# Kernel tuning notes

Hardware: AMD Instinct MI355X
Metric: run time of the kernel (lower is better)

Reference implementation:

```python
import jax, jax.numpy as jnp
import numpy as np

B, S, D, H, HID = 8192, 16, 128, 8, 1024
DH = D // H  # 16
GCN, NUMF = 40, 103
EPS = 1e-5

def _make_pe():
    pos = np.arange(S, dtype=np.float64)[:, None]
    i = np.arange(D, dtype=np.float64)[None, :]
    pe = pos / np.power(10000.0, (i // 2 * 2.0) / D)
    pe[:, 0::2] = np.sin(pe[:, 0::2])
    pe[:, 1::2] = np.cos(pe[:, 1::2])
    return jnp.asarray(pe, dtype=jnp.float32)  # [S, D]

PE = _make_pe()

def setup_inputs() -> dict:
    key = jax.random.key(0)
    ks = jax.random.split(key, 16)
    rn = lambda k, shape, s=0.02: (jax.random.normal(k, shape, jnp.float32) * s)
    return {
        "x": jax.random.normal(ks[0], (B, S, D), jnp.float32),
        "gcn_i": jax.random.normal(ks[1], (B, GCN), jnp.float32),
        "num": jax.random.normal(ks[2], (B, NUMF), jnp.float32),
        # two independent encoder layers, params stacked on leading dim
        "Wq": rn(ks[3], (2, D, D)), "bq": jnp.zeros((2, D), jnp.float32),
        "Wk": rn(ks[4], (2, D, D)), "bk": jnp.zeros((2, D), jnp.float32),
        "Wv": rn(ks[5], (2, D, D)), "bv": jnp.zeros((2, D), jnp.float32),
        "Wo": rn(ks[6], (2, D, D)), "bo": jnp.zeros((2, D), jnp.float32),
        "ln1_g": jnp.ones((2, D), jnp.float32), "ln1_b": jnp.zeros((2, D), jnp.float32),
        "W1": rn(ks[7], (2, D, HID)), "b1": jnp.zeros((2, HID), jnp.float32),
        "W2": rn(ks[8], (2, HID, D)), "b2": jnp.zeros((2, D), jnp.float32),
        "ln2_g": jnp.ones((2, D), jnp.float32), "ln2_b": jnp.zeros((2, D), jnp.float32),
        # head
        "Wn": rn(ks[9], (NUMF, D)), "bnum": jnp.zeros((D,), jnp.float32),
        "bn_gamma": jnp.ones((D,), jnp.float32), "bn_beta": jnp.zeros((D,), jnp.float32),
        "Wf": rn(ks[10], (S * D + GCN + D, 1)), "bf": jnp.zeros((1,), jnp.float32),
    }

def _ln(x, g, b):
    m = x.mean(-1, keepdims=True)
    v = ((x - m) ** 2).mean(-1, keepdims=True)
    return (x - m) * jax.lax.rsqrt(v + EPS) * g + b

def reference(x, gcn_i, num, Wq, bq, Wk, bk, Wv, bv, Wo, bo, ln1_g, ln1_b,
              W1, b1, W2, b2, ln2_g, ln2_b, Wn, bnum, bn_gamma, bn_beta, Wf, bf):
    out = x + PE  # positional encoding (dropout = identity in eval)
    scale = DH ** -0.5
    for l in range(2):
        # NOTE: original uses a raw .view(B*H, -1, DH) (no transpose) -- faithful reshape
        q = (out @ Wq[l] + bq[l]).reshape(B * H, S, DH)
        k = (out @ Wk[l] + bk[l]).reshape(B * H, S, DH)
        v = (out @ Wv[l] + bv[l]).reshape(B * H, S, DH)
        attn = jax.nn.softmax(jnp.einsum('nsd,ntd->nst', q, k) * scale, axis=-1)
        ctx = jnp.einsum('nst,ntd->nsd', attn, v).reshape(B, S, D)
        h = _ln(ctx @ Wo[l] + bo[l] + out, ln1_g[l], ln1_b[l])
        ff = jax.nn.relu(h @ W1[l] + b1[l]) @ W2[l] + b2[l]
        out = _ln(ff + h, ln2_g[l], ln2_b[l])
    flat = out.reshape(B, S * D)  # [B, 2048]
    n = num @ Wn + bnum  # [B, 128]
    # BatchNorm1d, training-mode forward (biased batch variance)
    mu = n.mean(0)
    var = ((n - mu) ** 2).mean(0)
    n = (n - mu) * jax.lax.rsqrt(var + EPS) * bn_gamma + bn_beta
    p = jnp.concatenate([flat, gcn_i, n], axis=-1)  # [B, 2216]
    return jax.nn.sigmoid(p @ Wf + bf)
```

## Files before the change

kernel.cpp:

```cpp
#include <hip/hip_runtime.h>
#include <hip/hip_bf16.h>
#include <math.h>

#define B_SZ   8192
#define S_SZ   16
#define D_SZ   128
#define HID_SZ 1024
#define NUMF_SZ 103
#define GCN_SZ 40
#define G_B    4
#define NBLK   (B_SZ / G_B)
#define STRD   136

typedef short bh8 __attribute__((ext_vector_type(8)));
typedef float fx4 __attribute__((ext_vector_type(4)));

__device__ __forceinline__ fx4 mfma16(bh8 a, bh8 b, fx4 c) {
    return __builtin_amdgcn_mfma_f32_16x16x32_bf16(a, b, c, 0, 0, 0);
}

__device__ __forceinline__ unsigned short f2b(float f) {
    unsigned u = __float_as_uint(f);
    return (unsigned short)((u + 0x7fffu + ((u >> 16) & 1u)) >> 16);
}
__device__ __forceinline__ float bu2f(unsigned short u) {
    return __uint_as_float(((unsigned)u) << 16);
}

__global__ __launch_bounds__(256) void prep_weights(
    const float* __restrict__ Wq, const float* __restrict__ Wk,
    const float* __restrict__ Wv, const float* __restrict__ Wo,
    const float* __restrict__ W1, const float* __restrict__ W2,
    unsigned short* __restrict__ WswQ, unsigned short* __restrict__ WswK,
    unsigned short* __restrict__ WswV, unsigned short* __restrict__ WswO,
    unsigned short* __restrict__ Wsw1, unsigned short* __restrict__ Wsw2,
    float* __restrict__ PEt)
{
    int i = blockIdx.x * 256 + threadIdx.x;
    if (i < 2048) {
        int s = i >> 7, c = i & 127;
        float expo = (float)((c >> 1) * 2) * (1.0f / 128.0f);
        float denom = powf(10000.0f, expo);
        float ang = (float)s / denom;
        PEt[i] = (c & 1) ? cosf(ang) : sinf(ang);
    }
    if (i < 2 * 16384) {
        int l = i >> 14, r = i & 16383;
        int nt = r >> 11, ks = (r >> 9) & 3, lane = (r >> 3) & 63, e = r & 7;
        int k = ks * 32 + (lane >> 4) * 8 + e;
        int n = nt * 16 + (lane & 15);
        int s = l * 16384 + k * 128 + n;
        WswQ[i] = f2b(Wq[s]); WswK[i] = f2b(Wk[s]);
        WswV[i] = f2b(Wv[s]); WswO[i] = f2b(Wo[s]);
    }
    {
        int l = i >> 17, r = i & 131071;
        int nt = r >> 11, ks = (r >> 9) & 3, lane = (r >> 3) & 63, e = r & 7;
        int k = ks * 32 + (lane >> 4) * 8 + e;
        int n = nt * 16 + (lane & 15);
        Wsw1[i] = f2b(W1[l * 131072 + k * 1024 + n]);
    }
    {
        int l = i >> 17, r = i & 131071;
        int nt = r >> 14, kt = (r >> 9) & 31, lane = (r >> 3) & 63, e = r & 7;
        int k = kt * 32 + (lane >> 4) * 8 + e;
        int n = nt * 16 + (lane & 15);
        Wsw2[i] = f2b(W2[l * 131072 + k * 128 + n]);
    }
}

__global__ __launch_bounds__(256, 2) void encoder_fused(
    const float* __restrict__ x, const float* __restrict__ gcn,
    const float* __restrict__ bq, const float* __restrict__ bk,
    const float* __restrict__ bv, const float* __restrict__ bo,
    const float* __restrict__ ln1g, const float* __restrict__ ln1b,
    const float* __restrict__ b1, const float* __restrict__ b2p,
    const float* __restrict__ ln2g, const float* __restrict__ ln2b,
    const float* __restrict__ Wf,
    const unsigned short* __restrict__ WswQ, const unsigned short* __restrict__ WswK,
    const unsigned short* __restrict__ WswV, const unsigned short* __restrict__ WswO,
    const unsigned short* __restrict__ Wsw1, const unsigned short* __restrict__ Wsw2,
    const float* __restrict__ PEt,
    float* __restrict__ acc1)
{
    __shared__ unsigned short ACT[64][STRD];
    __shared__ unsigned short Qb[64][STRD];
    __shared__ unsigned short Kb[64][STRD];
    __shared__ unsigned short Vb[64][STRD];
    __shared__ float LNp[64][4][2];
    __shared__ float LNs[64][2];

    const int t = threadIdx.x;
    const int w = t >> 6, lane = t & 63;
    const int q = lane >> 4, ln = lane & 15;
    const int bbase = blockIdx.x * G_B;

    {
        const float4* xb = (const float4*)(x + (size_t)bbase * 2048);
        const float4* pe4 = (const float4*)PEt;
#pragma unroll
        for (int i = 0; i < 8; ++i) {
            int f4 = i * 256 + t;
            float4 xv = xb[f4];
            float4 pv = pe4[f4 & 511];
            int flat = f4 * 4;
            int row = flat >> 7, col = flat & 127;
            ushort4 pk = {f2b(xv.x + pv.x), f2b(xv.y + pv.y),
                          f2b(xv.z + pv.z), f2b(xv.w + pv.w)};
            *(ushort4*)&ACT[row][col] = pk;
        }
    }
    __syncthreads();

    for (int l = 0; l < 2; ++l) {
        {
            bh8 afr[4][4];
#pragma unroll
            for (int mt = 0; mt < 4; ++mt)
#pragma unroll
                for (int ks = 0; ks < 4; ++ks)
                    afr[mt][ks] = *(const bh8*)&ACT[mt * 16 + ln][ks * 32 + q * 8];
            const unsigned short* Wm[3] = {WswQ + l * 16384, WswK + l * 16384, WswV + l * 16384};
            const float* bias3[3] = {bq + l * 128, bk + l * 128, bv + l * 128};
#pragma unroll
            for (int mtx = 0; mtx < 3; ++mtx) {
                unsigned short (*dst)[STRD] = (mtx == 0) ? Qb : (mtx == 1) ? Kb : Vb;
#pragma unroll
                for (int i2 = 0; i2 < 2; ++i2) {
                    int nt = w * 2 + i2;
                    bh8 wfr[4];
#pragma unroll
                    for (int ks = 0; ks < 4; ++ks)
                        wfr[ks] = *(const bh8*)(Wm[mtx] + ((nt * 4 + ks) * 64 + lane) * 8);
                    int n = nt * 16 + ln;
                    float bb = bias3[mtx][n];
#pragma unroll
                    for (int mt = 0; mt < 4; ++mt) {
                        fx4 acc = {0.f, 0.f, 0.f, 0.f};
#pragma unroll
                        for (int ks = 0; ks < 4; ++ks) acc = mfma16(afr[mt][ks], wfr[ks], acc);
#pragma unroll
                        for (int r2 = 0; r2 < 4; ++r2)
                            dst[mt * 16 + q * 4 + r2][n] = f2b(acc[r2] + bb);
                    }
                }
            }
        }
        __syncthreads();

        {
            int base = w * 16;
            int g = lane >> 3, u0 = (lane & 7) * 2;
            float qr[2][16];
#pragma unroll
            for (int h = 0; h < 2; ++h) {
                int u = u0 + h;
                int qsr = base + 2 * g + (u >> 3), qc = (u & 7) * 16;
                bh8 a0 = *(const bh8*)&Qb[qsr][qc];
                bh8 a1 = *(const bh8*)&Qb[qsr][qc + 8];
#pragma unroll
                for (int e = 0; e < 8; ++e) {
                    qr[h][e] = bu2f((unsigned short)a0[e]);
                    qr[h][8 + e] = bu2f((unsigned short)a1[e]);
                }
            }
            float p[2][16];
#pragma unroll
            for (int tp = 0; tp < 16; ++tp) {
                int ksr = base + 2 * g + (tp >> 3), kc = (tp & 7) * 16;
                bh8 k0 = *(const bh8*)&Kb[ksr][kc];
                bh8 k1 = *(const bh8*)&Kb[ksr][kc + 8];
                float d0 = 0.f, d1 = 0.f;
#pragma unroll
                for (int e = 0; e < 8; ++e) {
                    float kv = bu2f((unsigned short)k0[e]);
                    d0 = fmaf(qr[0][e], kv, d0); d1 = fmaf(qr[1][e], kv, d1);
                }
#pragma unroll
                for (int e = 0; e < 8; ++e) {
                    float kv = bu2f((unsigned short)k1[e]);
                    d0 = fmaf(qr[0][8 + e], kv, d0); d1 = fmaf(qr[1][8 + e], kv, d1);
                }
                p[0][tp] = d0 * 0.25f; p[1][tp] = d1 * 0.25f;
            }
#pragma unroll
            for (int h = 0; h < 2; ++h) {
                float mx = -1e30f;
#pragma unroll
                for (int tp = 0; tp < 16; ++tp) mx = fmaxf(mx, p[h][tp]);
                float sum = 0.f;
#pragma unroll
                for (int tp = 0; tp < 16; ++tp) { p[h][tp] = __expf(p[h][tp] - mx); sum += p[h][tp]; }
                float is = 1.0f / sum;
#pragma unroll
                for (int tp = 0; tp < 16; ++tp) p[h][tp] *= is;
            }
            float ctx[2][16];
#pragma unroll
            for (int h = 0; h < 2; ++h)
#pragma unroll
                for (int e = 0; e < 16; ++e) ctx[h][e] = 0.f;
#pragma unroll
            for (int tp = 0; tp < 16; ++tp) {
                int vsr = base + 2 * g + (tp >> 3), vc = (tp & 7) * 16;
                bh8 v0 = *(const bh8*)&Vb[vsr][vc];
                bh8 v1 = *(const bh8*)&Vb[vsr][vc + 8];
#pragma unroll
                for (int e = 0; e < 8; ++e) {
                    float vv = bu2f((unsigned short)v0[e]);
                    ctx[0][e] = fmaf(p[0][tp], vv, ctx[0][e]);
                    ctx[1][e] = fmaf(p[1][tp], vv, ctx[1][e]);
                }
#pragma unroll
                for (int e = 0; e < 8; ++e) {
                    float vv = bu2f((unsigned short)v1[e]);
                    ctx[0][8 + e] = fmaf(p[0][tp], vv, ctx[0][8 + e]);
                    ctx[1][8 + e] = fmaf(p[1][tp], vv, ctx[1][8 + e]);
                }
            }
#pragma unroll
            for (int h = 0; h < 2; ++h) {
                int u = u0 + h;
                int s = base + 2 * g + (u >> 3), dc = (u & 7) * 16;
                bh8 c0, c1;
#pragma unroll
                for (int e = 0; e < 8; ++e) {
                    c0[e] = (short)f2b(ctx[h][e]);
                    c1[e] = (short)f2b(ctx[h][8 + e]);
                }
                *(bh8*)&Qb[s][dc] = c0;
                *(bh8*)&Qb[s][dc + 8] = c1;
            }
        }
        __syncthreads();

        fx4 Cv[2][4];
        {
            bh8 cfr[4][4];
#pragma unroll
            for (int mt = 0; mt < 4; ++mt)
#pragma unroll
                for (int ks = 0; ks < 4; ++ks)
                    cfr[mt][ks] = *(const bh8*)&Qb[mt * 16 + ln][ks * 32 + q * 8];
#pragma unroll
            for (int i2 = 0; i2 < 2; ++i2) {
                int nt = w * 2 + i2, n = nt * 16 + ln;
                bh8 wfr[4];
#pragma unroll
                for (int ks = 0; ks < 4; ++ks)
                    wfr[ks] = *(const bh8*)(WswO + l * 16384 + ((nt * 4 + ks) * 64 + lane) * 8);
                float bb = bo[l * 128 + n];
#pragma unroll
                for (int mt = 0; mt < 4; ++mt) {
                    fx4 acc = {0.f, 0.f, 0.f, 0.f};
#pragma unroll
                    for (int ks = 0; ks < 4; ++ks) acc = mfma16(cfr[mt][ks], wfr[ks], acc);
#pragma unroll
                    for (int r2 = 0; r2 < 4; ++r2)
                        Cv[i2][mt][r2] = acc[r2] + bb +
                            bu2f(ACT[mt * 16 + q * 4 + r2][n]);
                }
            }
        }
#pragma unroll
        for (int mt = 0; mt < 4; ++mt) {
            float s4[4], v4[4];
#pragma unroll
            for (int r2 = 0; r2 < 4; ++r2) {
                float a0 = Cv[0][mt][r2], a1 = Cv[1][mt][r2];
                float s = a0 + a1, v = a0 * a0 + a1 * a1;
#pragma unroll
                for (int m = 1; m < 16; m <<= 1) { s += __shfl_xor(s, m); v += __shfl_xor(v, m); }
                s4[r2] = s; v4[r2] = v;
            }
            if (ln < 8)
                LNp[mt * 16 + q * 4 + (ln >> 1)][w][ln & 1] = (ln & 1) ? v4[ln >> 1] : s4[ln >> 1];
        }
        __syncthreads();
        if (t < 64) {
            float s = LNp[t][0][0] + LNp[t][1][0] + LNp[t][2][0] + LNp[t][3][0];
            float v = LNp[t][0][1] + LNp[t][1][1] + LNp[t][2][1] + LNp[t][3][1];
            float mean = s * (1.0f / 128.0f);
            LNs[t][0] = mean;
            LNs[t][1] = rsqrtf(v * (1.0f / 128.0f) - mean * mean + 1e-5f);
        }
        __syncthreads();
#pragma unroll
        for (int i2 = 0; i2 < 2; ++i2) {
            int n = (w * 2 + i2) * 16 + ln;
            float gg = ln1g[l * 128 + n], be = ln1b[l * 128 + n];
#pragma unroll
            for (int mt = 0; mt < 4; ++mt)
#pragma unroll
                for (int r2 = 0; r2 < 4; ++r2) {
                    int row = mt * 16 + q * 4 + r2;
                    Kb[row][n] = f2b((Cv[i2][mt][r2] - LNs[row][0]) * LNs[row][1] * gg + be);
                }
        }
        __syncthreads();

        bh8 hfr[4][4];
#pragma unroll
        for (int mt = 0; mt < 4; ++mt)
#pragma unroll
            for (int ks = 0; ks < 4; ++ks)
                hfr[mt][ks] = *(const bh8*)&Kb[mt * 16 + ln][ks * 32 + q * 8];
        fx4 f2a[2][4];
#pragma unroll
        for (int i2 = 0; i2 < 2; ++i2)
#pragma unroll
            for (int mt = 0; mt < 4; ++mt) f2a[i2][mt] = fx4{0.f, 0.f, 0.f, 0.f};
        for (int ch = 0; ch < 8; ++ch) {
            bh8 w1fr[2][4];
#pragma unroll
            for (int i2 = 0; i2 < 2; ++i2) {
                int ntg = ch * 8 + w * 2 + i2;
#pragma unroll
                for (int ks = 0; ks < 4; ++ks)
                    w1fr[i2][ks] = *(const bh8*)(Wsw1 + l * 131072 + ((ntg * 4 + ks) * 64 + lane) * 8);
            }
#pragma unroll
            for (int mt = 0; mt < 4; ++mt) {
#pragma unroll
                for (int i2 = 0; i2 < 2; ++i2) {
                    fx4 acc = {0.f, 0.f, 0.f, 0.f};
#pragma unroll
                    for (int ks = 0; ks < 4; ++ks) acc = mfma16(hfr[mt][ks], w1fr[i2][ks], acc);
                    int nl = (w * 2 + i2) * 16 + ln;
                    float bb = b1[l * HID_SZ + ch * 128 + nl];
#pragma unroll
                    for (int r2 = 0; r2 < 4; ++r2) {
                        float vv = acc[r2] + bb;
                        Qb[mt * 16 + q * 4 + r2][nl] = f2b(vv > 0.f ? vv : 0.f);
                    }
                }
            }
            __syncthreads();
            bh8 w2fr[2][4];
#pragma unroll
            for (int i2 = 0; i2 < 2; ++i2)
#pragma unroll
                for (int ks = 0; ks < 4; ++ks)
                    w2fr[i2][ks] = *(const bh8*)(Wsw2 + l * 131072 +
                        (((w * 2 + i2) * 32 + ch * 4 + ks) * 64 + lane) * 8);
#pragma unroll
            for (int mt = 0; mt < 4; ++mt) {
                bh8 ffr[4];
#pragma unroll
                for (int ks = 0; ks < 4; ++ks)
                    ffr[ks] = *(const bh8*)&Qb[mt * 16 + ln][ks * 32 + q * 8];
#pragma unroll
                for (int i2 = 0; i2 < 2; ++i2)
#pragma unroll
                    for (int ks = 0; ks < 4; ++ks)
                        f2a[i2][mt] = mfma16(ffr[ks], w2fr[i2][ks], f2a[i2][mt]);
            }
            __syncthreads();
        }
        fx4 Cv2[2][4];
#pragma unroll
        for (int i2 = 0; i2 < 2; ++i2) {
            int n = (w * 2 + i2) * 16 + ln;
            float bb = b2p[l * 128 + n];
#pragma unroll
            for (int mt = 0; mt < 4; ++mt)
#pragma unroll
                for (int r2 = 0; r2 < 4; ++r2)
                    Cv2[i2][mt][r2] = f2a[i2][mt][r2] + bb +
                        bu2f(Kb[mt * 16 + q * 4 + r2][n]);
        }
#pragma unroll
        for (int mt = 0; mt < 4; ++mt) {
            float s4[4], v4[4];
#pragma unroll
            for (int r2 = 0; r2 < 4; ++r2) {
                float a0 = Cv2[0][mt][r2], a1 = Cv2[1][mt][r2];
                float s = a0 + a1, v = a0 * a0 + a1 * a1;
#pragma unroll
                for (int m = 1; m < 16; m <<= 1) { s += __shfl_xor(s, m); v += __shfl_xor(v, m); }
                s4[r2] = s; v4[r2] = v;
            }
            if (ln < 8)
                LNp[mt * 16 + q * 4 + (ln >> 1)][w][ln & 1] = (ln & 1) ? v4[ln >> 1] : s4[ln >> 1];
        }
        __syncthreads();
        if (t < 64) {
            float s = LNp[t][0][0] + LNp[t][1][0] + LNp[t][2][0] + LNp[t][3][0];
            float v = LNp[t][0][1] + LNp[t][1][1] + LNp[t][2][1] + LNp[t][3][1];
            float mean = s * (1.0f / 128.0f);
            LNs[t][0] = mean;
            LNs[t][1] = rsqrtf(v * (1.0f / 128.0f) - mean * mean + 1e-5f);
        }
        __syncthreads();
#pragma unroll
        for (int i2 = 0; i2 < 2; ++i2) {
            int n = (w * 2 + i2) * 16 + ln;
            float gg = ln2g[l * 128 + n], be = ln2b[l * 128 + n];
#pragma unroll
            for (int mt = 0; mt < 4; ++mt)
#pragma unroll
                for (int r2 = 0; r2 < 4; ++r2) {
                    int row = mt * 16 + q * 4 + r2;
                    ACT[row][n] = f2b((Cv2[i2][mt][r2] - LNs[row][0]) * LNs[row][1] * gg + be);
                }
        }
        __syncthreads();
    }

    {
        int bg = bbase + w;
        float part = 0.f;
        int srow = lane >> 2, c0 = (lane & 3) * 32;
#pragma unroll
        for (int i = 0; i < 4; ++i) {
            bh8 av = *(const bh8*)&ACT[w * 16 + srow][c0 + i * 8];
            int fl = srow * 128 + c0 + i * 8;
#pragma unroll
            for (int e = 0; e < 8; ++e)
                part = fmaf(bu2f((unsigned short)av[e]), Wf[fl + e], part);
        }
        if (lane < GCN_SZ)
            part = fmaf(gcn[(size_t)bg * GCN_SZ + lane], Wf[2048 + lane], part);
#pragma unroll
        for (int off = 32; off; off >>= 1) part += __shfl_xor(part, off);
        if (lane == 0) acc1[bg] = part;
    }
}

__global__ __launch_bounds__(256) void num_stats_kernel(
    const float* __restrict__ num, const float* __restrict__ Wn,
    const float* __restrict__ bnum,
    float* __restrict__ ssum, float* __restrict__ ssq)
{
    __shared__ float NUM[16][NUMF_SZ + 1];
    __shared__ float cred[4][128];
    const int t = threadIdx.x;
    const int b0 = blockIdx.x * 16;
    const int j = t & 127, sg = t >> 7, s0 = sg * 8;

    for (int idx = t; idx < 16 * NUMF_SZ; idx += 256) {
        int r = idx / NUMF_SZ, f = idx - r * NUMF_SZ;
        NUM[r][f] = num[(size_t)(b0 + r) * NUMF_SZ + f];
    }
    __syncthreads();

    float acc[8];
    float bnv = bnum[j];
#pragma unroll
    for (int r = 0; r < 8; ++r) acc[r] = bnv;
    for (int f = 0; f < NUMF_SZ; ++f) {
        float w = Wn[f * 128 + j];
#pragma unroll
        for (int r = 0; r < 8; ++r) acc[r] = fmaf(NUM[s0 + r][f], w, acc[r]);
    }
    float lsum = 0.f, lsq = 0.f;
#pragma unroll
    for (int r = 0; r < 8; ++r) {
        lsum += acc[r];
        lsq = fmaf(acc[r], acc[r], lsq);
    }
    cred[sg][j] = lsum;
    cred[2 + sg][j] = lsq;
    __syncthreads();
    if (sg == 0) atomicAdd(&ssum[j], cred[0][j] + cred[1][j]);
    else         atomicAdd(&ssq[j],  cred[2][j] + cred[3][j]);
}

__global__ __launch_bounds__(128) void final_kernel(
    const float* __restrict__ num, const float* __restrict__ Wn,
    const float* __restrict__ bnum,
    const float* __restrict__ ssum, const float* __restrict__ ssq,
    const float* __restrict__ gamma, const float* __restrict__ beta,
    const float* __restrict__ Wf, const float* __restrict__ bfin,
    const float* __restrict__ acc1, float* __restrict__ out)
{
    const int b = blockIdx.x, jj = threadIdx.x;
    __shared__ float red2[2];
    __shared__ float NUMr[NUMF_SZ];
    if (jj < NUMF_SZ) NUMr[jj] = num[(size_t)b * NUMF_SZ + jj];
    __syncthreads();

    float nv = bnum[jj];
    for (int f = 0; f < NUMF_SZ; ++f)
        nv = fmaf(NUMr[f], Wn[f * 128 + jj], nv);

    float mean = ssum[jj] * (1.0f / (float)B_SZ);
    float var = ssq[jj] * (1.0f / (float)B_SZ) - mean * mean;
    float bnv = (nv - mean) * rsqrtf(var + 1e-5f) * gamma[jj] + beta[jj];
    float v = bnv * Wf[2088 + jj];
#pragma unroll
    for (int o = 32; o; o >>= 1) v += __shfl_down(v, o);
    if ((jj & 63) == 0) red2[jj >> 6] = v;
    __syncthreads();
    if (jj == 0) {
        float z = acc1[b] + red2[0] + red2[1] + bfin[0];
        out[b] = 1.0f / (1.0f + __expf(-z));
    }
}

extern "C" void kernel_launch(void* const* d_in, const int* in_sizes, int n_in,
                              void* d_out, int out_size, void* d_ws, size_t ws_size,
                              hipStream_t stream)
{
    const float* x    = (const float*)d_in[0];
    const float* gcn  = (const float*)d_in[1];
    const float* num  = (const float*)d_in[2];
    const float* Wq   = (const float*)d_in[3];
    const float* bq   = (const float*)d_in[4];
    const float* Wk   = (const float*)d_in[5];
    const float* bk   = (const float*)d_in[6];
    const float* Wv   = (const float*)d_in[7];
    const float* bv   = (const float*)d_in[8];
    const float* Wo   = (const float*)d_in[9];
    const float* bo   = (const float*)d_in[10];
    const float* ln1g = (const float*)d_in[11];
    const float* ln1b = (const float*)d_in[12];
    const float* W1   = (const float*)d_in[13];
    const float* b1   = (const float*)d_in[14];
    const float* W2   = (const float*)d_in[15];
    const float* b2p  = (const float*)d_in[16];
    const float* ln2g = (const float*)d_in[17];
    const float* ln2b = (const float*)d_in[18];
    const float* Wn   = (const float*)d_in[19];
    const float* bnum = (const float*)d_in[20];
    const float* bng  = (const float*)d_in[21];
    const float* bnb  = (const float*)d_in[22];
    const float* Wf   = (const float*)d_in[23];
    const float* bfin = (const float*)d_in[24];

    float* acc1 = (float*)d_ws;
    float* ssum = acc1 + B_SZ;
    float* ssq  = ssum + 128;
    unsigned short* wb = (unsigned short*)((char*)d_ws + 40960);
    unsigned short* WswQ = wb;
    unsigned short* WswK = wb + 32768;
    unsigned short* WswV = wb + 65536;
    unsigned short* WswO = wb + 98304;
    unsigned short* Wsw1 = wb + 131072;
    unsigned short* Wsw2 = wb + 393216;
    float* PEt = (float*)((char*)d_ws + 40960 + 1310720);

    hipMemsetAsync(ssum, 0, 2 * 128 * sizeof(float), stream);
    prep_weights<<<1024, 256, 0, stream>>>(Wq, Wk, Wv, Wo, W1, W2,
        WswQ, WswK, WswV, WswO, Wsw1, Wsw2, PEt);
    encoder_fused<<<NBLK, 256, 0, stream>>>(x, gcn, bq, bk, bv, bo,
        ln1g, ln1b, b1, b2p, ln2g, ln2b, Wf,
        WswQ, WswK, WswV, WswO, Wsw1, Wsw2, PEt, acc1);
    num_stats_kernel<<<B_SZ / 16, 256, 0, stream>>>(num, Wn, bnum, ssum, ssq);
    final_kernel<<<B_SZ, 128, 0, stream>>>(num, Wn, bnum, ssum, ssq, bng, bnb,
        Wf, bfin, acc1, (float*)d_out);
}
```

Before: 491.1 us.

## Double encoder block to 512 threads, one N-tile per wave; batch final kernel rows

The fused encoder now runs 8 waves per block, each owning one 16-column N tile instead of two, and attention splits into one head-row per thread. The LayerNorm partial reductions and the final dot-product reduction widen to cover 8 waves. The final kernel now processes 8 batch rows per block so each Wn load is reused across rows. The aim is more waves in flight to hide latency and fewer tiny blocks, at the cost of extra synchronisation and a launch bound that may force register spilling.

```diff
diff --git a/kernel.cpp b/kernel.cpp
--- a/kernel.cpp
+++ b/kernel.cpp
@@ -69,7 +69,7 @@
     }
 }
 
-__global__ __launch_bounds__(256, 2) void encoder_fused(
+__global__ __launch_bounds__(512, 4) void encoder_fused(
     const float* __restrict__ x, const float* __restrict__ gcn,
     const float* __restrict__ bq, const float* __restrict__ bk,
     const float* __restrict__ bv, const float* __restrict__ bo,
@@ -87,20 +87,22 @@
     __shared__ unsigned short Qb[64][STRD];
     __shared__ unsigned short Kb[64][STRD];
     __shared__ unsigned short Vb[64][STRD];
-    __shared__ float LNp[64][4][2];
+    __shared__ float LNp[64][8][2];
     __shared__ float LNs[64][2];
+    __shared__ float redH[8];
 
     const int t = threadIdx.x;
     const int w = t >> 6, lane = t & 63;
     const int q = lane >> 4, ln = lane & 15;
     const int bbase = blockIdx.x * G_B;
+    const int n = w * 16 + ln;
 
     {
         const float4* xb = (const float4*)(x + (size_t)bbase * 2048);
         const float4* pe4 = (const float4*)PEt;
 #pragma unroll
-        for (int i = 0; i < 8; ++i) {
-            int f4 = i * 256 + t;
+        for (int i = 0; i < 4; ++i) {
+            int f4 = i * 512 + t;
             float4 xv = xb[f4];
             float4 pv = pe4[f4 & 511];
             int flat = f4 * 4;
@@ -125,116 +127,87 @@
 #pragma unroll
             for (int mtx = 0; mtx < 3; ++mtx) {
                 unsigned short (*dst)[STRD] = (mtx == 0) ? Qb : (mtx == 1) ? Kb : Vb;
-#pragma unroll
-                for (int i2 = 0; i2 < 2; ++i2) {
-                    int nt = w * 2 + i2;
-                    bh8 wfr[4];
-#pragma unroll
-                    for (int ks = 0; ks < 4; ++ks)
-                        wfr[ks] = *(const bh8*)(Wm[mtx] + ((nt * 4 + ks) * 64 + lane) * 8);
-                    int n = nt * 16 + ln;
-                    float bb = bias3[mtx][n];
-#pragma unroll
-                    for (int mt = 0; mt < 4; ++mt) {
-                        fx4 acc = {0.f, 0.f, 0.f, 0.f};
-#pragma unroll
-                        for (int ks = 0; ks < 4; ++ks) acc = mfma16(afr[mt][ks], wfr[ks], acc);
-#pragma unroll
-                        for (int r2 = 0; r2 < 4; ++r2)
-                            dst[mt * 16 + q * 4 + r2][n] = f2b(acc[r2] + bb);
-                    }
+                bh8 wfr[4];
+#pragma unroll
+                for (int ks = 0; ks < 4; ++ks)
+                    wfr[ks] = *(const bh8*)(Wm[mtx] + ((w * 4 + ks) * 64 + lane) * 8);
+                float bb = bias3[mtx][n];
+#pragma unroll
+                for (int mt = 0; mt < 4; ++mt) {
+                    fx4 acc = {0.f, 0.f, 0.f, 0.f};
+#pragma unroll
+                    for (int ks = 0; ks < 4; ++ks) acc = mfma16(afr[mt][ks], wfr[ks], acc);
+#pragma unroll
+                    for (int r2 = 0; r2 < 4; ++r2)
+                        dst[mt * 16 + q * 4 + r2][n] = f2b(acc[r2] + bb);
                 }
             }
         }
         __syncthreads();
 
         {
-            int base = w * 16;
-            int g = lane >> 3, u0 = (lane & 7) * 2;
-            float qr[2][16];
-#pragma unroll
-            for (int h = 0; h < 2; ++h) {
-                int u = u0 + h;
-                int qsr = base + 2 * g + (u >> 3), qc = (u & 7) * 16;
+            int base = (w >> 1) * 16;
+            int g = (w & 1) * 4 + q;
+            int u = ln;
+            int qsr = base + 2 * g + (u >> 3), qc = (u & 7) * 16;
+            float qr[16];
+            {
                 bh8 a0 = *(const bh8*)&Qb[qsr][qc];
                 bh8 a1 = *(const bh8*)&Qb[qsr][qc + 8];
 #pragma unroll
                 for (int e = 0; e < 8; ++e) {
-                    qr[h][e] = bu2f((unsigned short)a0[e]);
-                    qr[h][8 + e] = bu2f((unsigned short)a1[e]);
+                    qr[e] = bu2f((unsigned short)a0[e]);
+                    qr[8 + e] = bu2f((unsigned short)a1[e]);
                 }
             }
-            float p[2][16];
+            float p[16];
 #pragma unroll
             for (int tp = 0; tp < 16; ++tp) {
                 int ksr = base + 2 * g + (tp >> 3), kc = (tp & 7) * 16;
                 bh8 k0 = *(const bh8*)&Kb[ksr][kc];
                 bh8 k1 = *(const bh8*)&Kb[ksr][kc + 8];
-                float d0 = 0.f, d1 = 0.f;
-#pragma unroll
-                for (int e = 0; e < 8; ++e) {
-                    float kv = bu2f((unsigned short)k0[e]);
-                    d0 = fmaf(qr[0][e], kv, d0); d1 = fmaf(qr[1][e], kv, d1);
-                }
-#pragma unroll
-                for (int e = 0; e < 8; ++e) {
-                    float kv = bu2f((unsigned short)k1[e]);
-                    d0 = fmaf(qr[0][8 + e], kv, d0); d1 = fmaf(qr[1][8 + e], kv, d1);
-                }
-                p[0][tp] = d0 * 0.25f; p[1][tp] = d1 * 0.25f;
-            }
-#pragma unroll
-            for (int h = 0; h < 2; ++h) {
-                float mx = -1e30f;
-#pragma unroll
-                for (int tp = 0; tp < 16; ++tp) mx = fmaxf(mx, p[h][tp]);
-                float sum = 0.f;
-#pragma unroll
-                for (int tp = 0; tp < 16; ++tp) { p[h][tp] = __expf(p[h][tp] - mx); sum += p[h][tp]; }
-                float is = 1.0f / sum;
-#pragma unroll
-                for (int tp = 0; tp < 16; ++tp) p[h][tp] *= is;
-            }
-            float ctx[2][16];
-#pragma unroll
-            for (int h = 0; h < 2; ++h)
-#pragma unroll
-                for (int e = 0; e < 16; ++e) ctx[h][e] = 0.f;
+                float d0 = 0.f;
+#pragma unroll
+                for (int e = 0; e < 8; ++e) d0 = fmaf(qr[e], bu2f((unsigned short)k0[e]), d0);
+#pragma unroll
+                for (int e = 0; e < 8; ++e) d0 = fmaf(qr[8 + e], bu2f((unsigned short)k1[e]), d0);
+                p[tp] = d0 * 0.25f;
+            }
+            float mx = -1e30f;
+#pragma unroll
+            for (int tp = 0; tp < 16; ++tp) mx = fmaxf(mx, p[tp]);
+            float sum = 0.f;
+#pragma unroll
+            for (int tp = 0; tp < 16; ++tp) { p[tp] = __expf(p[tp] - mx); sum += p[tp]; }
+            float is = 1.0f / sum;
+#pragma unroll
+            for (int tp = 0; tp < 16; ++tp) p[tp] *= is;
+            float ctx[16];
+#pragma unroll
+            for (int e = 0; e < 16; ++e) ctx[e] = 0.f;
 #pragma unroll
             for (int tp = 0; tp < 16; ++tp) {
                 int vsr = base + 2 * g + (tp >> 3), vc = (tp & 7) * 16;
                 bh8 v0 = *(const bh8*)&Vb[vsr][vc];
                 bh8 v1 = *(const bh8*)&Vb[vsr][vc + 8];
 #pragma unroll
-                for (int e = 0; e < 8; ++e) {
-                    float vv = bu2f((unsigned short)v0[e]);
-                    ctx[0][e] = fmaf(p[0][tp], vv, ctx[0][e]);
-                    ctx[1][e] = fmaf(p[1][tp], vv, ctx[1][e]);
-                }
-#pragma unroll
-                for (int e = 0; e < 8; ++e) {
-                    float vv = bu2f((unsigned short)v1[e]);
-                    ctx[0][8 + e] = fmaf(p[0][tp], vv, ctx[0][8 + e]);
-                    ctx[1][8 + e] = fmaf(p[1][tp], vv, ctx[1][8 + e]);
-                }
-            }
-#pragma unroll
-            for (int h = 0; h < 2; ++h) {
-                int u = u0 + h;
-                int s = base + 2 * g + (u >> 3), dc = (u & 7) * 16;
-                bh8 c0, c1;
-#pragma unroll
-                for (int e = 0; e < 8; ++e) {
-                    c0[e] = (short)f2b(ctx[h][e]);
-                    c1[e] = (short)f2b(ctx[h][8 + e]);
-                }
-                *(bh8*)&Qb[s][dc] = c0;
-                *(bh8*)&Qb[s][dc + 8] = c1;
-            }
-        }
-        __syncthreads();
-
-        fx4 Cv[2][4];
+                for (int e = 0; e < 8; ++e) ctx[e] = fmaf(p[tp], bu2f((unsigned short)v0[e]), ctx[e]);
+#pragma unroll
+                for (int e = 0; e < 8; ++e) ctx[8 + e] = fmaf(p[tp], bu2f((unsigned short)v1[e]), ctx[8 + e]);
+            }
+            __syncthreads();
+            bh8 c0, c1;
+#pragma unroll
+            for (int e = 0; e < 8; ++e) {
+                c0[e] = (short)f2b(ctx[e]);
+                c1[e] = (short)f2b(ctx[8 + e]);
+            }
+            *(bh8*)&Qb[qsr][qc] = c0;
+            *(bh8*)&Qb[qsr][qc + 8] = c1;
+        }
+        __syncthreads();
+
+        fx4 Cv[4];
         {
             bh8 cfr[4][4];
 #pragma unroll
@@ -242,24 +215,19 @@
 #pragma unroll
                 for (int ks = 0; ks < 4; ++ks)
                     cfr[mt][ks] = *(const bh8*)&Qb[mt * 16 + ln][ks * 32 + q * 8];
-#pragma unroll
-            for (int i2 = 0; i2 < 2; ++i2) {
-                int nt = w * 2 + i2, n = nt * 16 + ln;
-                bh8 wfr[4];
-#pragma unroll
-                for (int ks = 0; ks < 4; ++ks)
-                    wfr[ks] = *(const bh8*)(WswO + l * 16384 + ((nt * 4 + ks) * 64 + lane) * 8);
-                float bb = bo[l * 128 + n];
-#pragma unroll
-                for (int mt = 0; mt < 4; ++mt) {
-                    fx4 acc = {0.f, 0.f, 0.f, 0.f};
-#pragma unroll
-                    for (int ks = 0; ks < 4; ++ks) acc = mfma16(cfr[mt][ks], wfr[ks], acc);
-#pragma unroll
-                    for (int r2 = 0; r2 < 4; ++r2)
-                        Cv[i2][mt][r2] = acc[r2] + bb +
-                            bu2f(ACT[mt * 16 + q * 4 + r2][n]);
-                }
+            bh8 wfr[4];
+#pragma unroll
+            for (int ks = 0; ks < 4; ++ks)
+                wfr[ks] = *(const bh8*)(WswO + l * 16384 + ((w * 4 + ks) * 64 + lane) * 8);
+            float bb = bo[l * 128 + n];
+#pragma unroll
+            for (int mt = 0; mt < 4; ++mt) {
+                fx4 acc = {0.f, 0.f, 0.f, 0.f};
+#pragma unroll
+                for (int ks = 0; ks < 4; ++ks) acc = mfma16(cfr[mt][ks], wfr[ks], acc);
+#pragma unroll
+                for (int r2 = 0; r2 < 4; ++r2)
+                    Cv[mt][r2] = acc[r2] + bb + bu2f(ACT[mt * 16 + q * 4 + r2][n]);
             }
         }
 #pragma unroll
@@ -267,8 +235,8 @@
             float s4[4], v4[4];
 #pragma unroll
             for (int r2 = 0; r2 < 4; ++r2) {
-                float a0 = Cv[0][mt][r2], a1 = Cv[1][mt][r2];
-                float s = a0 + a1, v = a0 * a0 + a1 * a1;
+                float a0 = Cv[mt][r2];
+                float s = a0, v = a0 * a0;
 #pragma unroll
                 for (int m = 1; m < 16; m <<= 1) { s += __shfl_xor(s, m); v += __shfl_xor(v, m); }
                 s4[r2] = s; v4[r2] = v;
@@ -278,23 +246,22 @@
         }
         __syncthreads();
         if (t < 64) {
-            float s = LNp[t][0][0] + LNp[t][1][0] + LNp[t][2][0] + LNp[t][3][0];
-            float v = LNp[t][0][1] + LNp[t][1][1] + LNp[t][2][1] + LNp[t][3][1];
+            float s = 0.f, v = 0.f;
+#pragma unroll
+            for (int ww = 0; ww < 8; ++ww) { s += LNp[t][ww][0]; v += LNp[t][ww][1]; }
             float mean = s * (1.0f / 128.0f);
             LNs[t][0] = mean;
             LNs[t][1] = rsqrtf(v * (1.0f / 128.0f) - mean * mean + 1e-5f);
         }
         __syncthreads();
-#pragma unroll
-        for (int i2 = 0; i2 < 2; ++i2) {
-            int n = (w * 2 + i2) * 16 + ln;
+        {
             float gg = ln1g[l * 128 + n], be = ln1b[l * 128 + n];
 #pragma unroll
             for (int mt = 0; mt < 4; ++mt)
 #pragma unroll
                 for (int r2 = 0; r2 < 4; ++r2) {
                     int row = mt * 16 + q * 4 + r2;
-                    Kb[row][n] = f2b((Cv[i2][mt][r2] - LNs[row][0]) * LNs[row][1] * gg + be);
+                    Kb[row][n] = f2b((Cv[mt][r2] - LNs[row][0]) * LNs[row][1] * gg + be);
                 }
         }
         __syncthreads();
@@ -305,44 +272,35 @@
 #pragma unroll
             for (int ks = 0; ks < 4; ++ks)
                 hfr[mt][ks] = *(const bh8*)&Kb[mt * 16 + ln][ks * 32 + q * 8];
-        fx4 f2a[2][4];
-#pragma unroll
-        for (int i2 = 0; i2 < 2; ++i2)
-#pragma unroll
-            for (int mt = 0; mt < 4; ++mt) f2a[i2][mt] = fx4{0.f, 0.f, 0.f, 0.f};
+        fx4 f2a[4];
+#pragma unroll
+        for (int mt = 0; mt < 4; ++mt) f2a[mt] = fx4{0.f, 0.f, 0.f, 0.f};
         for (int ch = 0; ch < 8; ++ch) {
-            bh8 w1fr[2][4];
-#pragma unroll
-            for (int i2 = 0; i2 < 2; ++i2) {
-                int ntg = ch * 8 + w * 2 + i2;
+            bh8 w1fr[4];
+            {
+                int ntg = ch * 8 + w;
 #pragma unroll
                 for (int ks = 0; ks < 4; ++ks)
-                    w1fr[i2][ks] = *(const bh8*)(Wsw1 + l * 131072 + ((ntg * 4 + ks) * 64 + lane) * 8);
-            }
+                    w1fr[ks] = *(const bh8*)(Wsw1 + l * 131072 + ((ntg * 4 + ks) * 64 + lane) * 8);
+            }
+            float bb = b1[l * HID_SZ + ch * 128 + n];
 #pragma unroll
             for (int mt = 0; mt < 4; ++mt) {
-#pragma unroll
-                for (int i2 = 0; i2 < 2; ++i2) {
-                    fx4 acc = {0.f, 0.f, 0.f, 0.f};
-#pragma unroll
-                    for (int ks = 0; ks < 4; ++ks) acc = mfma16(hfr[mt][ks], w1fr[i2][ks], acc);
-                    int nl = (w * 2 + i2) * 16 + ln;
-                    float bb = b1[l * HID_SZ + ch * 128 + nl];
-#pragma unroll
-                    for (int r2 = 0; r2 < 4; ++r2) {
-                        float vv = acc[r2] + bb;
-                        Qb[mt * 16 + q * 4 + r2][nl] = f2b(vv > 0.f ? vv : 0.f);
-                    }
+                fx4 acc = {0.f, 0.f, 0.f, 0.f};
+#pragma unroll
+                for (int ks = 0; ks < 4; ++ks) acc = mfma16(hfr[mt][ks], w1fr[ks], acc);
+#pragma unroll
+                for (int r2 = 0; r2 < 4; ++r2) {
+                    float vv = acc[r2] + bb;
+                    Qb[mt * 16 + q * 4 + r2][n] = f2b(vv > 0.f ? vv : 0.f);
                 }
             }
             __syncthreads();
-            bh8 w2fr[2][4];
-#pragma unroll
-            for (int i2 = 0; i2 < 2; ++i2)
-#pragma unroll
-                for (int ks = 0; ks < 4; ++ks)
-                    w2fr[i2][ks] = *(const bh8*)(Wsw2 + l * 131072 +
-                        (((w * 2 + i2) * 32 + ch * 4 + ks) * 64 + lane) * 8);
+            bh8 w2fr[4];
+#pragma unroll
+            for (int ks = 0; ks < 4; ++ks)
+                w2fr[ks] = *(const bh8*)(Wsw2 + l * 131072 +
+                    ((w * 32 + ch * 4 + ks) * 64 + lane) * 8);
 #pragma unroll
             for (int mt = 0; mt < 4; ++mt) {
                 bh8 ffr[4];
@@ -350,32 +308,27 @@
                 for (int ks = 0; ks < 4; ++ks)
                     ffr[ks] = *(const bh8*)&Qb[mt * 16 + ln][ks * 32 + q * 8];
 #pragma unroll
-                for (int i2 = 0; i2 < 2; ++i2)
-#pragma unroll
-                    for (int ks = 0; ks < 4; ++ks)
-                        f2a[i2][mt] = mfma16(ffr[ks], w2fr[i2][ks], f2a[i2][mt]);
+                for (int ks = 0; ks < 4; ++ks)
+                    f2a[mt] = mfma16(ffr[ks], w2fr[ks], f2a[mt]);
             }
             __syncthreads();
         }
-        fx4 Cv2[2][4];
-#pragma unroll
-        for (int i2 = 0; i2 < 2; ++i2) {
-            int n = (w * 2 + i2) * 16 + ln;
+        fx4 Cv2[4];
+        {
             float bb = b2p[l * 128 + n];
 #pragma unroll
             for (int mt = 0; mt < 4; ++mt)
 #pragma unroll
                 for (int r2 = 0; r2 < 4; ++r2)
-                    Cv2[i2][mt][r2] = f2a[i2][mt][r2] + bb +
-                        bu2f(Kb[mt * 16 + q * 4 + r2][n]);
+                    Cv2[mt][r2] = f2a[mt][r2] + bb + bu2f(Kb[mt * 16 + q * 4 + r2][n]);
         }
 #pragma unroll
         for (int mt = 0; mt < 4; ++mt) {
             float s4[4], v4[4];
 #pragma unroll
             for (int r2 = 0; r2 < 4; ++r2) {
-                float a0 = Cv2[0][mt][r2], a1 = Cv2[1][mt][r2];
-                float s = a0 + a1, v = a0 * a0 + a1 * a1;
+                float a0 = Cv2[mt][r2];
+                float s = a0, v = a0 * a0;
 #pragma unroll
                 for (int m = 1; m < 16; m <<= 1) { s += __shfl_xor(s, m); v += __shfl_xor(v, m); }
                 s4[r2] = s; v4[r2] = v;
@@ -385,46 +338,48 @@
         }
         __syncthreads();
         if (t < 64) {
-            float s = LNp[t][0][0] + LNp[t][1][0] + LNp[t][2][0] + LNp[t][3][0];
-            float v = LNp[t][0][1] + LNp[t][1][1] + LNp[t][2][1] + LNp[t][3][1];
+            float s = 0.f, v = 0.f;
+#pragma unroll
+            for (int ww = 0; ww < 8; ++ww) { s += LNp[t][ww][0]; v += LNp[t][ww][1]; }
             float mean = s * (1.0f / 128.0f);
             LNs[t][0] = mean;
             LNs[t][1] = rsqrtf(v * (1.0f / 128.0f) - mean * mean + 1e-5f);
         }
         __syncthreads();
-#pragma unroll
-        for (int i2 = 0; i2 < 2; ++i2) {
-            int n = (w * 2 + i2) * 16 + ln;
+        {
             float gg = ln2g[l * 128 + n], be = ln2b[l * 128 + n];
 #pragma unroll
             for (int mt = 0; mt < 4; ++mt)
 #pragma unroll
                 for (int r2 = 0; r2 < 4; ++r2) {
                     int row = mt * 16 + q * 4 + r2;
-                    ACT[row][n] = f2b((Cv2[i2][mt][r2] - LNs[row][0]) * LNs[row][1] * gg + be);
+                    ACT[row][n] = f2b((Cv2[mt][r2] - LNs[row][0]) * LNs[row][1] * gg + be);
                 }
         }
         __syncthreads();
     }
 
     {
-        int bg = bbase + w;
+        int bl = w >> 1;
+        int bg = bbase + bl;
         float part = 0.f;
-        int srow = lane >> 2, c0 = (lane & 3) * 32;
-#pragma unroll
-        for (int i = 0; i < 4; ++i) {
-            bh8 av = *(const bh8*)&ACT[w * 16 + srow][c0 + i * 8];
+        int srow = lane >> 2, c0 = (lane & 3) * 32 + (w & 1) * 16;
+#pragma unroll
+        for (int i = 0; i < 2; ++i) {
+            bh8 av = *(const bh8*)&ACT[bl * 16 + srow][c0 + i * 8];
             int fl = srow * 128 + c0 + i * 8;
 #pragma unroll
             for (int e = 0; e < 8; ++e)
                 part = fmaf(bu2f((unsigned short)av[e]), Wf[fl + e], part);
         }
-        if (lane < GCN_SZ)
+        if ((w & 1) == 0 && lane < GCN_SZ)
             part = fmaf(gcn[(size_t)bg * GCN_SZ + lane], Wf[2048 + lane], part);
 #pragma unroll
         for (int off = 32; off; off >>= 1) part += __shfl_xor(part, off);
-        if (lane == 0) acc1[bg] = part;
-    }
+        if (lane == 0) redH[w] = part;
+    }
+    __syncthreads();
+    if (t < G_B) acc1[bbase + t] = redH[2 * t] + redH[2 * t + 1];
 }
 
 __global__ __launch_bounds__(256) void num_stats_kernel(
@@ -474,27 +429,43 @@
     const float* __restrict__ Wf, const float* __restrict__ bfin,
     const float* __restrict__ acc1, float* __restrict__ out)
 {
-    const int b = blockIdx.x, jj = threadIdx.x;
-    __shared__ float red2[2];
-    __shared__ float NUMr[NUMF_SZ];
-    if (jj < NUMF_SZ) NUMr[jj] = num[(size_t)b * NUMF_SZ + jj];
+    const int b0 = blockIdx.x * 8, jj = threadIdx.x;
+    __shared__ float NUMr[8][NUMF_SZ];
+    __shared__ float redF[2][8];
+    for (int idx = jj; idx < 8 * NUMF_SZ; idx += 128) {
+        int r = idx / NUMF_SZ, f = idx - r * NUMF_SZ;
+        NUMr[r][f] = num[(size_t)(b0 + r) * NUMF_SZ + f];
+    }
     __syncthreads();
 
-    float nv = bnum[jj];
-    for (int f = 0; f < NUMF_SZ; ++f)
-        nv = fmaf(NUMr[f], Wn[f * 128 + jj], nv);
-
+    float nv[8];
+    float bn = bnum[jj];
+#pragma unroll
+    for (int r = 0; r < 8; ++r) nv[r] = bn;
+    for (int f = 0; f < NUMF_SZ; ++f) {
+        float wv = Wn[f * 128 + jj];
+#pragma unroll
+        for (int r = 0; r < 8; ++r) nv[r] = fmaf(NUMr[r][f], wv, nv[r]);
+    }
     float mean = ssum[jj] * (1.0f / (float)B_SZ);
     float var = ssq[jj] * (1.0f / (float)B_SZ) - mean * mean;
-    float bnv = (nv - mean) * rsqrtf(var + 1e-5f) * gamma[jj] + beta[jj];
-    float v = bnv * Wf[2088 + jj];
-#pragma unroll
-    for (int o = 32; o; o >>= 1) v += __shfl_down(v, o);
-    if ((jj & 63) == 0) red2[jj >> 6] = v;
+    float scale = rsqrtf(var + 1e-5f) * gamma[jj];
+    float bet = beta[jj];
+    float wf = Wf[2088 + jj];
+    float v[8];
+#pragma unroll
+    for (int r = 0; r < 8; ++r) v[r] = ((nv[r] - mean) * scale + bet) * wf;
+#pragma unroll
+    for (int off = 32; off; off >>= 1)
+#pragma unroll
+        for (int r = 0; r < 8; ++r) v[r] += __shfl_xor(v[r], off);
+    if ((jj & 63) == 0)
+#pragma unroll
+        for (int r = 0; r < 8; ++r) redF[jj >> 6][r] = v[r];
     __syncthreads();
-    if (jj == 0) {
-        float z = acc1[b] + red2[0] + red2[1] + bfin[0];
-        out[b] = 1.0f / (1.0f + __expf(-z));
+    if (jj < 8) {
+        float z = acc1[b0 + jj] + redF[0][jj] + redF[1][jj] + bfin[0];
+        out[b0 + jj] = 1.0f / (1.0f + __expf(-z));
     }
 }
 
@@ -543,10 +514,10 @@
     hipMemsetAsync(ssum, 0, 2 * 128 * sizeof(float), stream);
     prep_weights<<<1024, 256, 0, stream>>>(Wq, Wk, Wv, Wo, W1, W2,
         WswQ, WswK, WswV, WswO, Wsw1, Wsw2, PEt);
-    encoder_fused<<<NBLK, 256, 0, stream>>>(x, gcn, bq, bk, bv, bo,
+    encoder_fused<<<NBLK, 512, 0, stream>>>(x, gcn, bq, bk, bv, bo,
         ln1g, ln1b, b1, b2p, ln2g, ln2b, Wf,
         WswQ, WswK, WswV, WswO, Wsw1, Wsw2, PEt, acc1);
     num_stats_kernel<<<B_SZ / 16, 256, 0, stream>>>(num, Wn, bnum, ssum, ssq);
-    final_kernel<<<B_SZ, 128, 0, stream>>>(num, Wn, bnum, ssum, ssq, bng, bnb,
+    final_kernel<<<B_SZ / 8, 128, 0, stream>>>(num, Wn, bnum, ssum, ssq, bng, bnb,
         Wf, bfin, acc1, (float*)d_out);
 }
```

New measurement: 551.3 us. 1.12x slower.
